# Performance work log

Measured on AMD Instinct MI355X. Metric: run time of the kernel, lower is better.

The kernel has to match this reference:

```python
import jax, jax.numpy as jnp
import numpy as np

D_MODEL = 1024
NUM_HEADS = 16
D_K = D_MODEL // NUM_HEADS
B, S = 2, 2048
NEG = -1e9


def setup_inputs() -> dict:
    key = jax.random.key(0)
    ks = jax.random.split(key, 12)
    sc = 1.0 / np.sqrt(D_MODEL)
    inp = {
        'Q': jax.random.normal(ks[0], (B, S, D_MODEL), jnp.float32),
        'K': jax.random.normal(ks[1], (B, S, D_MODEL), jnp.float32),
        'V': jax.random.normal(ks[2], (B, S, D_MODEL), jnp.float32),
        # causal additive mask: 1.0 above diagonal -> scores += mask * -1e9
        'mask': jnp.triu(jnp.ones((S, S), jnp.float32), k=1),
        'Wq': jax.random.normal(ks[3], (D_MODEL, D_MODEL), jnp.float32) * sc,
        'bq': jnp.zeros((D_MODEL,), jnp.float32),
        'Wk': jax.random.normal(ks[4], (D_MODEL, D_MODEL), jnp.float32) * sc,
        'bk': jnp.zeros((D_MODEL,), jnp.float32),
        'Wv': jax.random.normal(ks[5], (D_MODEL, D_MODEL), jnp.float32) * sc,
        'bv': jnp.zeros((D_MODEL,), jnp.float32),
        'Wo': jax.random.normal(ks[6], (D_MODEL, D_MODEL), jnp.float32) * sc,
        'bo': jnp.zeros((D_MODEL,), jnp.float32),
    }
    return inp


def _split_heads(x):
    # [B,S,D] -> [B,H,S,d_k]
    b, s, _ = x.shape
    return x.reshape(b, s, NUM_HEADS, D_K).transpose(0, 2, 1, 3)


def reference(Q, K, V, mask, Wq, bq, Wk, bk, Wv, bv, Wo, bo):
    # torch Linear: y = x @ W.T + b
    q = _split_heads(Q @ Wq.T + bq)  # [B,H,S,d_k]
    k = _split_heads(K @ Wk.T + bk)
    v = _split_heads(V @ Wv.T + bv)
    scores = jnp.einsum('bhqd,bhkd->bhqk', q, k) / np.sqrt(D_K)
    scores = scores + mask * NEG  # mask broadcasts over [B,H]
    probs = jax.nn.softmax(scores, axis=-1)
    attn = jnp.einsum('bhqk,bhkd->bhqd', probs, v)  # [B,H,S,d_k]
    attn = attn.transpose(0, 2, 1, 3).reshape(Q.shape[0], Q.shape[1], D_MODEL)
    return attn @ Wo.T + bo
```

## Files before the change

### kernel.cpp

```cpp
#include <hip/hip_runtime.h>
#include <cstdint>
#include <cstddef>

#define D_MODEL 1024
#define NHEADS  16
#define DK      64
#define BATCH   2
#define SEQ     2048
#define MTOT    (BATCH*SEQ)

typedef unsigned short u16;
typedef __attribute__((ext_vector_type(8))) __bf16 bf16x8;
typedef __attribute__((ext_vector_type(4))) float  f32x4;
typedef __attribute__((ext_vector_type(16))) float f32x16;
typedef __attribute__((ext_vector_type(4))) uint32_t u32x4;

#define QSCALE 0.18033688f

static __device__ __forceinline__ void gload16(const void* g, void* l) {
  __builtin_amdgcn_global_load_lds((const __attribute__((address_space(1))) void*)g,
                                   (__attribute__((address_space(3))) void*)l,
                                   16, 0, 0);
}

static __device__ __forceinline__ float bfu(u16 x) {
  union { uint32_t u; float f; } v; v.u = (uint32_t)x << 16; return v.f;
}

__global__ void cast_all_kernel(
    const float* __restrict__ Q, const float* __restrict__ K, const float* __restrict__ V,
    const float* __restrict__ Wq, const float* __restrict__ Wk,
    const float* __restrict__ Wv, const float* __restrict__ Wo,
    u16* __restrict__ dstX, u16* __restrict__ dstW) {
  constexpr int NX = MTOT * D_MODEL;
  constexpr int NW = D_MODEL * D_MODEL;
  const int i = (blockIdx.x * blockDim.x + threadIdx.x) * 4;
  const float* src;
  u16* dst;
  if (i < 3 * NX) {
    dst = dstX + i;
    src = (i < NX) ? Q + i : (i < 2 * NX) ? K + (i - NX) : V + (i - 2 * NX);
  } else {
    const int j = i - 3 * NX;
    dst = dstW + j;
    const int ws = j >> 20;
    const int jo = j & (NW - 1);
    src = (ws == 0) ? Wq + jo : (ws == 1) ? Wk + jo : (ws == 2) ? Wv + jo : Wo + jo;
  }
  float4 f = *reinterpret_cast<const float4*>(src);
  union { __bf16 h[4]; ushort4 s; } o;
  o.h[0] = (__bf16)f.x; o.h[1] = (__bf16)f.y; o.h[2] = (__bf16)f.z; o.h[3] = (__bf16)f.w;
  *reinterpret_cast<ushort4*>(dst) = o.s;
}

__global__ __launch_bounds__(256, 3) void gemm_qkv(
    const u16* __restrict__ A,
    const u16* __restrict__ W0, const u16* __restrict__ W1, const u16* __restrict__ W2,
    const float* __restrict__ b0, const float* __restrict__ b1, const float* __restrict__ b2,
    u16* __restrict__ out_q, u16* __restrict__ out_k, u16* __restrict__ out_v) {
  constexpr int K = 1024;
  constexpr int EP = 136;
  __shared__ __align__(16) u16 smem[128 * EP];
  u16* lA = smem;
  u16* lB = smem + 128 * 64;
  const int w = threadIdx.x >> 6, lane = threadIdx.x & 63;
  const int blockM = blockIdx.x * 128, blockN = blockIdx.y * 128;
  const int sel = blockIdx.x >> 5;
  const u16*  Bt   = sel == 0 ? W0 : (sel == 1 ? W1 : W2);
  const float* bias = sel == 0 ? b0 : (sel == 1 ? b1 : b2);
  const int wm = (w >> 1) * 64, wn = (w & 1) * 64;
  f32x4 acc[4][4] = {};
  for (int kt = 0; kt < K; kt += 64) {
#pragma unroll
    for (int it = 0; it < 4; ++it) {
      int rowb = w * 32 + it * 8;
      int row  = rowb + (lane >> 3);
      int cc   = (lane & 7) * 8;
      gload16(A  + (size_t)(blockM + row) * K + kt + cc, &lA[rowb * 64]);
      gload16(Bt + (size_t)(blockN + row) * K + kt + cc, &lB[rowb * 64]);
    }
    __syncthreads();
#pragma unroll
    for (int kc = 0; kc < 2; ++kc) {
      bf16x8 af[4], bfr[4];
#pragma unroll
      for (int i = 0; i < 4; ++i)
        af[i] = *(const bf16x8*)&lA[(wm + i * 16 + (lane & 15)) * 64 + kc * 32 + (lane >> 4) * 8];
#pragma unroll
      for (int j = 0; j < 4; ++j)
        bfr[j] = *(const bf16x8*)&lB[(wn + j * 16 + (lane & 15)) * 64 + kc * 32 + (lane >> 4) * 8];
#pragma unroll
      for (int i = 0; i < 4; ++i)
#pragma unroll
        for (int j = 0; j < 4; ++j)
          acc[i][j] = __builtin_amdgcn_mfma_f32_16x16x32_bf16(af[i], bfr[j], acc[i][j], 0, 0, 0);
    }
    __syncthreads();
  }
  if (sel == 2) {
#pragma unroll
    for (int i = 0; i < 4; ++i)
#pragma unroll
      for (int j = 0; j < 4; ++j) {
        int m0 = blockM + wm + i * 16 + (lane >> 4) * 4;
        int n  = blockN + wn + j * 16 + (lane & 15);
        int ml = m0 & (MTOT - 1);
        int b = ml >> 11, s = ml & (SEQ - 1), h = n >> 6, d = n & (DK - 1);
        union { __bf16 h4[4]; ushort4 s4; } st;
#pragma unroll
        for (int r = 0; r < 4; ++r) st.h4[r] = (__bf16)(acc[i][j][r] + bias[n]);
        *(ushort4*)&out_v[(((size_t)(b * NHEADS + h)) * DK + d) * SEQ + s] = st.s4;
      }
  } else {
#pragma unroll
    for (int i = 0; i < 4; ++i)
#pragma unroll
      for (int j = 0; j < 4; ++j) {
        int n = blockN + wn + j * 16 + (lane & 15);
        float bn = bias[n];
#pragma unroll
        for (int r = 0; r < 4; ++r) {
          float val = acc[i][j][r] + bn;
          if (sel == 0) val *= QSCALE;
          union { __bf16 h2; u16 u; } cv; cv.h2 = (__bf16)val;
          smem[(wm + i * 16 + (lane >> 4) * 4 + r) * EP + wn + j * 16 + (lane & 15)] = cv.u;
        }
      }
    __syncthreads();
    u16* outqk = sel ? out_k : out_q;
    const int t = threadIdx.x;
    const int seg = t & 15;
    const int h = (blockN >> 6) + (seg >> 3);
    const int d = (seg & 7) * 8;
#pragma unroll
    for (int pass = 0; pass < 8; ++pass) {
      const int row = pass * 16 + (t >> 4);
      u32x4 vdat = *(const u32x4*)&smem[row * EP + seg * 8];
      const int m = blockM + row;
      const int ml = m & (MTOT - 1);
      const int b = ml >> 11, s = ml & (SEQ - 1);
      *(u32x4*)&outqk[(((size_t)(b * NHEADS + h)) * SEQ + s) * DK + d] = vdat;
    }
  }
}

__global__ __launch_bounds__(256, 2) void gemm_out(
    const u16* __restrict__ A, const u16* __restrict__ Bt,
    const float* __restrict__ bias, float* __restrict__ outp) {
  constexpr int K = 1024, N = 1024;
  __shared__ __align__(16) u16 lA[64 * 64];
  __shared__ __align__(16) u16 lB[128 * 64];
  const int w = threadIdx.x >> 6, lane = threadIdx.x & 63;
  const int blockM = blockIdx.x * 64, blockN = blockIdx.y * 128;
  const int wm = (w >> 1) * 32, wn = (w & 1) * 64;
  f32x4 acc[2][4] = {};
  for (int kt = 0; kt < K; kt += 64) {
#pragma unroll
    for (int it = 0; it < 2; ++it) {
      int rowb = w * 16 + it * 8;
      int row  = rowb + (lane >> 3);
      int cc   = (lane & 7) * 8;
      gload16(A + (size_t)(blockM + row) * K + kt + cc, &lA[rowb * 64]);
    }
#pragma unroll
    for (int it = 0; it < 4; ++it) {
      int rowb = w * 32 + it * 8;
      int row  = rowb + (lane >> 3);
      int cc   = (lane & 7) * 8;
      gload16(Bt + (size_t)(blockN + row) * K + kt + cc, &lB[rowb * 64]);
    }
    __syncthreads();
#pragma unroll
    for (int kc = 0; kc < 2; ++kc) {
      bf16x8 af[2], bfr[4];
#pragma unroll
      for (int i = 0; i < 2; ++i)
        af[i] = *(const bf16x8*)&lA[(wm + i * 16 + (lane & 15)) * 64 + kc * 32 + (lane >> 4) * 8];
#pragma unroll
      for (int j = 0; j < 4; ++j)
        bfr[j] = *(const bf16x8*)&lB[(wn + j * 16 + (lane & 15)) * 64 + kc * 32 + (lane >> 4) * 8];
#pragma unroll
      for (int i = 0; i < 2; ++i)
#pragma unroll
        for (int j = 0; j < 4; ++j)
          acc[i][j] = __builtin_amdgcn_mfma_f32_16x16x32_bf16(af[i], bfr[j], acc[i][j], 0, 0, 0);
    }
    __syncthreads();
  }
#pragma unroll
  for (int i = 0; i < 2; ++i)
#pragma unroll
    for (int j = 0; j < 4; ++j)
#pragma unroll
      for (int r = 0; r < 4; ++r) {
        int m = blockM + wm + i * 16 + (lane >> 4) * 4 + r;
        int n = blockN + wn + j * 16 + (lane & 15);
        outp[(size_t)m * N + n] = acc[i][j][r] + bias[n];
      }
}

static __device__ __forceinline__ void stage_kv(
    const u16* kp, const u16* vp, int j0,
    u16* bufK, u16* bufV, int w, int lane) {
  const int rsub = lane >> 3;
  const int cl = ((lane & 7) ^ rsub) << 3;
#pragma unroll
  for (int it = 0; it < 2; ++it) {
    const int rowb = w * 16 + it * 8;
    gload16(kp + (size_t)(j0 + rowb + rsub) * DK + cl, bufK + rowb * 64);
    gload16(vp + (size_t)(rowb + rsub) * SEQ + j0 + cl, bufV + rowb * 64);
  }
}

__global__ __launch_bounds__(256) void attn_kernel(
    const u16* __restrict__ qh, const u16* __restrict__ kh,
    const u16* __restrict__ vt, u16* __restrict__ attnb,
    u16* __restrict__ pO, float2* __restrict__ pML) {
  __shared__ __align__(16) u16 lKV[2][2][64 * 64];
  const int w = threadIdx.x >> 6, lane = threadIdx.x & 63;
  const int q31 = lane & 31, h = lane >> 5;
  const int lid = blockIdx.x;
  const int xcd = lid & 7;
  const int idx = lid >> 3;
  const int p   = idx & 3;
  const int sraw = idx >> 2;
  const int s = 39 - sraw;
  const int bh = xcd * 4 + p;
  int qt, c, nch;
  if (s < 4)       { qt = s;                 c = 0;          nch = 1; }
  else if (s < 12) { int u = s - 4;  qt = 4 + (u >> 1); c = u & 1;  nch = 2; }
  else if (s < 24) { int u = s - 12; int q3 = u / 3; qt = 8 + q3; c = u - q3 * 3; nch = 3; }
  else             { int u = s - 24; qt = 12 + (u >> 2); c = u & 3; nch = 4; }
  const int nt_full = 2 * qt + 2;
  const int t_begin = c * 8;
  const int t_end   = min(t_begin + 8, nt_full);
  const int split   = nch > 1;
  const int b = bh >> 4, hd = bh & 15;
  const u16* qp = qh + (size_t)bh * SEQ * DK;
  const u16* kp = kh + (size_t)bh * SEQ * DK;
  const u16* vp = vt + (size_t)bh * DK * SEQ;

  const int qbase = qt * 128;
  const int qrow = qbase + w * 32 + q31;
  const int wave_max_row = qbase + w * 32 + 31;
  bf16x8 aq[4];
  const u16* qr = qp + (size_t)qrow * DK;
#pragma unroll
  for (int kc = 0; kc < 4; ++kc)
    aq[kc] = *(const bf16x8*)(qr + kc * 16 + h * 8);

  float m_run = -1e30f, l_run = 0.f;
  f32x16 oacc[2] = {};
  stage_kv(kp, vp, t_begin * 64, lKV[t_begin & 1][0], lKV[t_begin & 1][1], w, lane);

  for (int t = t_begin; t < t_end; ++t) {
    __syncthreads();
    const int cur = t & 1;
    if (t + 1 < t_end)
      stage_kv(kp, vp, (t + 1) * 64, lKV[cur ^ 1][0], lKV[cur ^ 1][1], w, lane);
    if (64 * t > wave_max_row) continue;
    const u16* bK = lKV[cur][0];
    const u16* bV = lKV[cur][1];

    f32x16 sacc[2] = {};
    __builtin_amdgcn_s_setprio(1);
#pragma unroll
    for (int kc = 0; kc < 4; ++kc)
#pragma unroll
      for (int jb = 0; jb < 2; ++jb) {
        const int rr = jb * 32 + q31;
        const int cc = kc * 2 + h;
        bf16x8 kf = *(const bf16x8*)&bK[rr * 64 + ((cc ^ (rr & 7)) << 3)];
        sacc[jb] = __builtin_amdgcn_mfma_f32_32x32x16_bf16(kf, aq[kc], sacc[jb], 0, 0, 0);
      }
    __builtin_amdgcn_s_setprio(0);

    float mx = -1e30f;
    const bool dg = (64 * t + 63) > (qbase + w * 32);
    if (dg) {
#pragma unroll
      for (int jb = 0; jb < 2; ++jb)
#pragma unroll
        for (int r = 0; r < 16; ++r) {
          float ss = sacc[jb][r];
          const int j = t * 64 + jb * 32 + (r & 3) + 8 * (r >> 2) + 4 * h;
          if (j > qrow) ss = -1e30f;
          sacc[jb][r] = ss;
          mx = fmaxf(mx, ss);
        }
    } else {
#pragma unroll
      for (int jb = 0; jb < 2; ++jb)
#pragma unroll
        for (int r = 0; r < 16; ++r) mx = fmaxf(mx, sacc[jb][r]);
    }
    mx = fmaxf(mx, __shfl_xor(mx, 32));
    if (__any(mx > m_run + 8.0f)) {
      const float mn = fmaxf(m_run, mx);
      const float alpha = __builtin_amdgcn_exp2f(m_run - mn);
      m_run = mn;
      l_run *= alpha;
#pragma unroll
      for (int db = 0; db < 2; ++db)
#pragma unroll
        for (int r = 0; r < 16; ++r) oacc[db][r] *= alpha;
    }
    float rs = 0.f;
#pragma unroll
    for (int jb = 0; jb < 2; ++jb)
#pragma unroll
      for (int r = 0; r < 16; ++r) {
        float e = __builtin_amdgcn_exp2f(sacc[jb][r] - m_run);
        sacc[jb][r] = e;
        rs += e;
      }
    rs += __shfl_xor(rs, 32);
    l_run += rs;

    uint32_t pk[2][4][2];
#pragma unroll
    for (int jb = 0; jb < 2; ++jb)
#pragma unroll
      for (int G = 0; G < 4; ++G)
#pragma unroll
        for (int u = 0; u < 2; ++u) {
          union { __bf16 h2[2]; uint32_t v; } cv;
          cv.h2[0] = (__bf16)sacc[jb][4 * G + 2 * u];
          cv.h2[1] = (__bf16)sacc[jb][4 * G + 2 * u + 1];
          pk[jb][G][u] = cv.v;
        }

#pragma unroll
    for (int jseg = 0; jseg < 4; ++jseg) {
      const int jb = jseg >> 1;
      const int G0 = (jseg & 1) * 2;
      const uint32_t s0 = h ? pk[jb][G0 + 1][0] : pk[jb][G0][0];
      const uint32_t s1 = h ? pk[jb][G0 + 1][1] : pk[jb][G0][1];
      const uint32_t e0 = h ? pk[jb][G0][0] : pk[jb][G0 + 1][0];
      const uint32_t e1 = h ? pk[jb][G0][1] : pk[jb][G0 + 1][1];
      const uint32_t f0 = (uint32_t)__shfl_xor((int)e0, 32);
      const uint32_t f1 = (uint32_t)__shfl_xor((int)e1, 32);
      union { u32x4 u; bf16x8 bvec; } pf;
      pf.u[0] = h ? f0 : s0;
      pf.u[1] = h ? f1 : s1;
      pf.u[2] = h ? s0 : f0;
      pf.u[3] = h ? s1 : f1;
      __builtin_amdgcn_s_setprio(1);
#pragma unroll
      for (int db = 0; db < 2; ++db) {
        const int rr = db * 32 + q31;
        const int cc = jseg * 2 + h;
        bf16x8 vf = *(const bf16x8*)&bV[rr * 64 + ((cc ^ (rr & 7)) << 3)];
        oacc[db] = __builtin_amdgcn_mfma_f32_32x32x16_bf16(vf, pf.bvec, oacc[db], 0, 0, 0);
      }
      __builtin_amdgcn_s_setprio(0);
    }
  }

  if (!split) {
    const float rl = 1.0f / l_run;
#pragma unroll
    for (int db = 0; db < 2; ++db)
#pragma unroll
      for (int G = 0; G < 4; ++G) {
        union { __bf16 h4[4]; ushort4 s4; } st;
#pragma unroll
        for (int e = 0; e < 4; ++e) st.h4[e] = (__bf16)(oacc[db][4 * G + e] * rl);
        *(ushort4*)&attnb[((size_t)(b * SEQ + qrow)) * D_MODEL + hd * 64 + db * 32 + 8 * G + 4 * h] = st.s4;
      }
  } else {
    const int pid = bh * 36 + (s - 4);
    u16* po = pO + (size_t)pid * 8192 + (size_t)(w * 32 + q31) * 64;
#pragma unroll
    for (int db = 0; db < 2; ++db)
#pragma unroll
      for (int G = 0; G < 4; ++G) {
        union { __bf16 h4[4]; ushort4 s4; } st;
#pragma unroll
        for (int e = 0; e < 4; ++e) st.h4[e] = (__bf16)oacc[db][4 * G + e];
        *(ushort4*)(po + db * 32 + 8 * G + 4 * h) = st.s4;
      }
    if (h == 0) {
      float2 ml; ml.x = m_run; ml.y = l_run;
      pML[(size_t)pid * 128 + w * 32 + q31] = ml;
    }
  }
}

__global__ __launch_bounds__(256) void attn_combine(
    const u16* __restrict__ pO, const float2* __restrict__ pML,
    u16* __restrict__ attnb) {
  const int blk = blockIdx.x;
  const int bh = blk / 12, qi = blk - (blk / 12) * 12;
  const int qt = 4 + qi;
  const int b = bh >> 4, h = bh & 15;
  int nch, sbase;
  if (qt < 8)       { nch = 2; sbase = 4 + (qt - 4) * 2; }
  else if (qt < 12) { nch = 3; sbase = 12 + (qt - 8) * 3; }
  else              { nch = 4; sbase = 24 + (qt - 12) * 4; }
  const int pbase = bh * 36 + (sbase - 4);
  const int t = threadIdx.x;
  const int c0 = (t & 3) * 16;

#pragma unroll
  for (int rp = 0; rp < 2; ++rp) {
    const int row = rp * 64 + (t >> 2);
    float m[4] = {-1e30f, -1e30f, -1e30f, -1e30f};
    float l[4] = {0.f, 0.f, 0.f, 0.f};
    float M = -1e30f;
#pragma unroll
    for (int i = 0; i < 4; ++i)
      if (i < nch) {
        float2 ml = pML[(size_t)(pbase + i) * 128 + row];
        m[i] = ml.x; l[i] = ml.y;
        M = fmaxf(M, ml.x);
      }
    float denom = 0.f, sc[4];
#pragma unroll
    for (int i = 0; i < 4; ++i) {
      sc[i] = __builtin_amdgcn_exp2f(m[i] - M);
      denom += l[i] * sc[i];
    }
    const float inv = 1.0f / denom;
    float out[16] = {};
#pragma unroll
    for (int i = 0; i < 4; ++i)
      if (i < nch) {
        const float scale = sc[i] * inv;
        const u16* pp = pO + (size_t)(pbase + i) * 8192 + row * 64 + c0;
        u32x4 d0 = *(const u32x4*)pp;
        u32x4 d1 = *(const u32x4*)(pp + 8);
#pragma unroll
        for (int k = 0; k < 4; ++k) {
          out[2 * k + 0] += scale * bfu((u16)(d0[k] & 0xffffu));
          out[2 * k + 1] += scale * bfu((u16)(d0[k] >> 16));
          out[8 + 2 * k + 0] += scale * bfu((u16)(d1[k] & 0xffffu));
          out[8 + 2 * k + 1] += scale * bfu((u16)(d1[k] >> 16));
        }
      }
    union { __bf16 h8[8]; u32x4 s; } o0, o1;
#pragma unroll
    for (int k = 0; k < 8; ++k) { o0.h8[k] = (__bf16)out[k]; o1.h8[k] = (__bf16)out[8 + k]; }
    u16* dst = attnb + ((size_t)(b * SEQ + qt * 128 + row)) * D_MODEL + h * 64 + c0;
    *(u32x4*)dst = o0.s;
    *(u32x4*)(dst + 8) = o1.s;
  }
}

extern "C" void kernel_launch(void* const* d_in, const int* in_sizes, int n_in,
                              void* d_out, int out_size, void* d_ws, size_t ws_size,
                              hipStream_t stream) {
  (void)in_sizes; (void)n_in; (void)out_size; (void)ws_size;
  const float* Q  = (const float*)d_in[0];
  const float* K  = (const float*)d_in[1];
  const float* V  = (const float*)d_in[2];
  const float* Wq = (const float*)d_in[4];
  const float* bq = (const float*)d_in[5];
  const float* Wk = (const float*)d_in[6];
  const float* bk = (const float*)d_in[7];
  const float* Wv = (const float*)d_in[8];
  const float* bv = (const float*)d_in[9];
  const float* Wo = (const float*)d_in[10];
  const float* bo = (const float*)d_in[11];

  char* ws = (char*)d_ws;
  size_t off = 0;
  auto carve = [&](size_t bytes) { char* p = ws + off; off += bytes; return p; };
  const size_t szX = (size_t)MTOT * D_MODEL * 2;
  const size_t szW = (size_t)D_MODEL * D_MODEL * 2;
  u16* Qb  = (u16*)carve(szX);
  u16* Kb  = (u16*)carve(szX);
  u16* Vb  = (u16*)carve(szX);
  u16* Wqb = (u16*)carve(szW);
  u16* Wkb = (u16*)carve(szW);
  u16* Wvb = (u16*)carve(szW);
  u16* Wob = (u16*)carve(szW);
  u16* qhB = (u16*)carve(szX);
  u16* khB = (u16*)carve(szX);
  u16* vtB = (u16*)carve(szX);
  u16* attnb = Qb;
  u16*    pO  = (u16*)Kb;
  float2* pML = (float2*)((char*)Kb + (size_t)19 * 1024 * 1024);
  (void)Wkb; (void)Wvb;

  const int nTot = 3 * MTOT * D_MODEL + 4 * D_MODEL * D_MODEL;
  cast_all_kernel<<<nTot / 1024, 256, 0, stream>>>(Q, K, V, Wq, Wk, Wv, Wo, Qb, Wqb);

  gemm_qkv<<<dim3(3 * MTOT / 128, D_MODEL / 128), 256, 0, stream>>>(
      Qb, Wqb, Wkb, Wvb, bq, bk, bv, qhB, khB, vtB);

  attn_kernel<<<1280, 256, 0, stream>>>(qhB, khB, vtB, attnb, pO, pML);

  attn_combine<<<384, 256, 0, stream>>>(pO, pML, attnb);

  gemm_out<<<dim3(MTOT / 64, D_MODEL / 128), 256, 0, stream>>>(attnb, Wob, bo, (float*)d_out);
}
```

Baseline: 124.3 us.

## Load K/V fragments directly from global memory instead of LDS double buffering

Removes the shared-memory double-buffered K/V staging, along with its per-tile __syncthreads, from the attention kernel. Each wave now reads its K and V MFMA fragments straight from global memory into registers, and the V loads are issued early so they overlap the softmax. This drops LDS traffic and block-wide barriers and frees LDS for occupancy. In exchange, the four waves now reload the same K/V tiles redundantly through cache, and global load latency is exposed with no prefetch across tiles.

```diff
diff --git a/kernel.cpp b/kernel.cpp
--- a/kernel.cpp
+++ b/kernel.cpp
@@ -199,24 +199,10 @@
       }
 }
 
-static __device__ __forceinline__ void stage_kv(
-    const u16* kp, const u16* vp, int j0,
-    u16* bufK, u16* bufV, int w, int lane) {
-  const int rsub = lane >> 3;
-  const int cl = ((lane & 7) ^ rsub) << 3;
-#pragma unroll
-  for (int it = 0; it < 2; ++it) {
-    const int rowb = w * 16 + it * 8;
-    gload16(kp + (size_t)(j0 + rowb + rsub) * DK + cl, bufK + rowb * 64);
-    gload16(vp + (size_t)(rowb + rsub) * SEQ + j0 + cl, bufV + rowb * 64);
-  }
-}
-
 __global__ __launch_bounds__(256) void attn_kernel(
     const u16* __restrict__ qh, const u16* __restrict__ kh,
     const u16* __restrict__ vt, u16* __restrict__ attnb,
     u16* __restrict__ pO, float2* __restrict__ pML) {
-  __shared__ __align__(16) u16 lKV[2][2][64 * 64];
   const int w = threadIdx.x >> 6, lane = threadIdx.x & 63;
   const int q31 = lane & 31, h = lane >> 5;
   const int lid = blockIdx.x;
@@ -251,29 +237,33 @@
 
   float m_run = -1e30f, l_run = 0.f;
   f32x16 oacc[2] = {};
-  stage_kv(kp, vp, t_begin * 64, lKV[t_begin & 1][0], lKV[t_begin & 1][1], w, lane);
 
   for (int t = t_begin; t < t_end; ++t) {
-    __syncthreads();
-    const int cur = t & 1;
-    if (t + 1 < t_end)
-      stage_kv(kp, vp, (t + 1) * 64, lKV[cur ^ 1][0], lKV[cur ^ 1][1], w, lane);
     if (64 * t > wave_max_row) continue;
-    const u16* bK = lKV[cur][0];
-    const u16* bV = lKV[cur][1];
+    const size_t j0 = (size_t)t * 64;
+
+    bf16x8 kf[4][2];
+#pragma unroll
+    for (int kc = 0; kc < 4; ++kc)
+#pragma unroll
+      for (int jb = 0; jb < 2; ++jb)
+        kf[kc][jb] = *(const bf16x8*)(kp + (j0 + jb * 32 + q31) * DK + (kc * 2 + h) * 8);
 
     f32x16 sacc[2] = {};
     __builtin_amdgcn_s_setprio(1);
 #pragma unroll
     for (int kc = 0; kc < 4; ++kc)
 #pragma unroll
-      for (int jb = 0; jb < 2; ++jb) {
-        const int rr = jb * 32 + q31;
-        const int cc = kc * 2 + h;
-        bf16x8 kf = *(const bf16x8*)&bK[rr * 64 + ((cc ^ (rr & 7)) << 3)];
-        sacc[jb] = __builtin_amdgcn_mfma_f32_32x32x16_bf16(kf, aq[kc], sacc[jb], 0, 0, 0);
-      }
+      for (int jb = 0; jb < 2; ++jb)
+        sacc[jb] = __builtin_amdgcn_mfma_f32_32x32x16_bf16(kf[kc][jb], aq[kc], sacc[jb], 0, 0, 0);
     __builtin_amdgcn_s_setprio(0);
+
+    bf16x8 vf[4][2];
+#pragma unroll
+    for (int jseg = 0; jseg < 4; ++jseg)
+#pragma unroll
+      for (int db = 0; db < 2; ++db)
+        vf[jseg][db] = *(const bf16x8*)(vp + (size_t)(db * 32 + q31) * SEQ + j0 + (jseg * 2 + h) * 8);
 
     float mx = -1e30f;
     const bool dg = (64 * t + 63) > (qbase + w * 32);
@@ -347,12 +337,8 @@
       pf.u[3] = h ? s1 : f1;
       __builtin_amdgcn_s_setprio(1);
 #pragma unroll
-      for (int db = 0; db < 2; ++db) {
-        const int rr = db * 32 + q31;
-        const int cc = jseg * 2 + h;
-        bf16x8 vf = *(const bf16x8*)&bV[rr * 64 + ((cc ^ (rr & 7)) << 3)];
-        oacc[db] = __builtin_amdgcn_mfma_f32_32x32x16_bf16(vf, pf.bvec, oacc[db], 0, 0, 0);
-      }
+      for (int db = 0; db < 2; ++db)
+        oacc[db] = __builtin_amdgcn_mfma_f32_32x32x16_bf16(vf[jseg][db], pf.bvec, oacc[db], 0, 0, 0);
       __builtin_amdgcn_s_setprio(0);
     }
   }
```

After: 170.7 us. +37.3%, slower.
